# Performance work log

Hardware: AMD Instinct MI355X
Metric: run time of the kernel (lower is better)

The kernel has to match this reference:

```python
import jax, jax.numpy as jnp
import numpy as np

B, S, D, K = 4, 8192, 512, 20


def setup_inputs() -> dict:
    key = jax.random.key(0)
    k1, k2, k3, k4 = jax.random.split(key, 4)
    std = 0.02  # _init_weights: normal(0, 0.02/sqrt(layer_idx+1)), layer_idx=0
    return {
        "x": jax.random.normal(k1, (B, S, D), dtype=jnp.float32),
        "positions": jax.random.normal(k2, (K, D), dtype=jnp.float32) * 0.2,
        "log_scales": jnp.log(1.0 + 0.5 * jax.random.uniform(k3, (K,), dtype=jnp.float32)),
        "amplitudes": 1.2 + 0.3 * jax.random.uniform(k4, (K,), dtype=jnp.float32),
        "w_v": jax.random.normal(jax.random.fold_in(key, 10), (D, D), dtype=jnp.float32) * std,
        "w_o": jax.random.normal(jax.random.fold_in(key, 11), (D, D), dtype=jnp.float32) * std,
    }


def reference(x, positions, log_scales, amplitudes, w_v, w_o):
    # Gaussian-splat RBF attention (token -> splat -> token routing).
    scales = jnp.exp(log_scales)  # [K]
    # squared distances ||x - c||^2 via expansion (avoids [B,S,K,D] tensor)
    x2 = jnp.sum(x * x, axis=-1, keepdims=True)           # [B,S,1]
    c2 = jnp.sum(positions * positions, axis=-1)          # [K]
    xc = jnp.einsum('bsd,kd->bsk', x, positions)          # [B,S,K]
    d2 = jnp.maximum(x2 - 2.0 * xc + c2, 0.0)             # [B,S,K]
    gauss = amplitudes * jnp.exp(-0.5 * d2 / (scales * scales))  # [B,S,K]
    attn = gauss / (jnp.sum(gauss, axis=-1, keepdims=True) + 1e-8)  # per-token normalize
    v = jnp.einsum('bsd,ed->bse', x, w_v)                 # token_value_proj (no bias)
    splat_states = jnp.einsum('bsk,bsd->bkd', attn, v)    # gather token values at splats
    out = jnp.einsum('bsk,bkd->bsd', attn, splat_states)  # scatter back to tokens
    return jnp.einsum('bsd,ed->bse', out, w_o)            # output_proj (dropout=eval identity)
```

## Files before the change

kernel.cpp:

```cpp
#include <hip/hip_runtime.h>
#include <hip/hip_bf16.h>

#define BB 4
#define SS 8192
#define DD 512
#define KK 20

__device__ __forceinline__ float dot4(float4 a, float4 b) {
  return a.x * b.x + a.y * b.y + a.z * b.z + a.w * b.w;
}

__global__ void k0_params(const float* __restrict__ pos,
                          const float* __restrict__ log_scales,
                          const float* __restrict__ amps,
                          float* __restrict__ params) {
  int k = blockIdx.x;
  int lane = threadIdx.x;
  float acc = 0.f;
  for (int d = lane; d < DD; d += 64) { float p = pos[k * DD + d]; acc += p * p; }
#pragma unroll
  for (int off = 32; off > 0; off >>= 1) acc += __shfl_xor(acc, off);
  if (lane == 0) {
    params[k] = acc;
    float s = __expf(log_scales[k]);
    params[KK + k] = 0.5f / (s * s);
    params[2 * KK + k] = amps[k];
  }
}

__global__ __launch_bounds__(256) void kA_attn(
    const float* __restrict__ x, const float* __restrict__ pos,
    const float* __restrict__ params, float* __restrict__ attn_g) {
  __shared__ float pos_s[KK * DD];
  __shared__ float prm_s[3 * KK];
  int tid = threadIdx.x;
  for (int i = tid; i < KK * DD / 4; i += 256)
    ((float4*)pos_s)[i] = ((const float4*)pos)[i];
  if (tid < 3 * KK) prm_s[tid] = params[tid];
  __syncthreads();

  int b = blockIdx.x >> 8;
  int c = blockIdx.x & 255;
  size_t row0 = (size_t)b * SS + (size_t)c * 32;
  int g = tid >> 4;
  int dsub = tid & 15;

  const float* xA = x + (row0 + g) * DD;
  const float* xB = xA + 16 * DD;

  float accA[KK], accB[KK], x2A = 0.f, x2B = 0.f;
#pragma unroll
  for (int k = 0; k < KK; ++k) { accA[k] = 0.f; accB[k] = 0.f; }

#pragma unroll 2
  for (int j = 0; j < 8; ++j) {
    int d0 = j * 64 + dsub * 4;
    float4 xa = *(const float4*)(xA + d0);
    float4 xb = *(const float4*)(xB + d0);
    x2A += dot4(xa, xa);
    x2B += dot4(xb, xb);
#pragma unroll
    for (int k = 0; k < KK; ++k) {
      float4 p = *(const float4*)(pos_s + k * DD + d0);
      accA[k] += dot4(xa, p);
      accB[k] += dot4(xb, p);
    }
  }

#pragma unroll
  for (int m = 1; m <= 8; m <<= 1) { x2A += __shfl_xor(x2A, m); x2B += __shfl_xor(x2B, m); }
#pragma unroll
  for (int k = 0; k < KK; ++k) {
#pragma unroll
    for (int m = 1; m <= 8; m <<= 1) {
      accA[k] += __shfl_xor(accA[k], m);
      accB[k] += __shfl_xor(accB[k], m);
    }
  }

  if (dsub == 0) {
    float gg[KK];
    float sum = 0.f;
#pragma unroll
    for (int k = 0; k < KK; ++k) {
      float d2 = fmaxf(x2A - 2.f * accA[k] + prm_s[k], 0.f);
      gg[k] = prm_s[2 * KK + k] * __expf(-prm_s[KK + k] * d2);
      sum += gg[k];
    }
    float inv = 1.f / (sum + 1e-8f);
    float* ar = attn_g + (row0 + g) * KK;
#pragma unroll
    for (int k = 0; k < KK; ++k) ar[k] = gg[k] * inv;

    sum = 0.f;
#pragma unroll
    for (int k = 0; k < KK; ++k) {
      float d2 = fmaxf(x2B - 2.f * accB[k] + prm_s[k], 0.f);
      gg[k] = prm_s[2 * KK + k] * __expf(-prm_s[KK + k] * d2);
      sum += gg[k];
    }
    inv = 1.f / (sum + 1e-8f);
    ar = attn_g + (row0 + g + 16) * KK;
#pragma unroll
    for (int k = 0; k < KK; ++k) ar[k] = gg[k] * inv;
  }
}

__global__ __launch_bounds__(256) void kB_scatter(
    const float* __restrict__ x, const float* __restrict__ attn,
    float* __restrict__ Mpart, int tpc) {
  int t = threadIdx.x;
  int c = blockIdx.x;
  int b = blockIdx.y;
  int cpb = gridDim.x;
  size_t row0 = (size_t)b * SS + (size_t)c * tpc;

  float2 Ml[KK];
#pragma unroll
  for (int k = 0; k < KK; ++k) Ml[k] = make_float2(0.f, 0.f);

  const float* xb = x + row0 * DD + 2 * t;
  const float* ab = attn + row0 * KK;
  for (int s = 0; s < tpc; ++s) {
    float2 xv = *(const float2*)(xb + (size_t)s * DD);
    const float4* ar4 = (const float4*)(ab + s * KK);
#pragma unroll
    for (int kk = 0; kk < KK / 4; ++kk) {
      float4 a4 = ar4[kk];
      Ml[4 * kk + 0].x += a4.x * xv.x; Ml[4 * kk + 0].y += a4.x * xv.y;
      Ml[4 * kk + 1].x += a4.y * xv.x; Ml[4 * kk + 1].y += a4.y * xv.y;
      Ml[4 * kk + 2].x += a4.z * xv.x; Ml[4 * kk + 2].y += a4.z * xv.y;
      Ml[4 * kk + 3].x += a4.w * xv.x; Ml[4 * kk + 3].y += a4.w * xv.y;
    }
  }
  float* mp = Mpart + ((size_t)b * cpb + c) * KK * DD + 2 * t;
#pragma unroll
  for (int k = 0; k < KK; ++k) *(float2*)(mp + (size_t)k * DD) = Ml[k];
}

__global__ __launch_bounds__(512) void k3f(
    const float* __restrict__ Mpart, const float* __restrict__ w_v,
    const float* __restrict__ w_o, float* __restrict__ ws2, int cpb) {
  __shared__ float m_s[DD];
  __shared__ float v_s[DD];
  int bk = blockIdx.x;
  int b = bk / KK, k = bk - b * KK;
  int e = threadIdx.x;

  const float* mp = Mpart + ((size_t)b * cpb) * KK * DD + (size_t)k * DD + e;
  float acc = 0.f;
#pragma unroll 8
  for (int c = 0; c < cpb; ++c) acc += mp[(size_t)c * KK * DD];
  m_s[e] = acc;
  __syncthreads();

  const float4* wr = (const float4*)(w_v + (size_t)e * DD);
  float a2 = 0.f;
#pragma unroll 4
  for (int j = 0; j < DD / 4; ++j) a2 += dot4(((const float4*)m_s)[j], wr[j]);
  v_s[e] = a2;
  __syncthreads();

  const float4* wr2 = (const float4*)(w_o + (size_t)e * DD);
  float a3 = 0.f;
#pragma unroll 4
  for (int j = 0; j < DD / 4; ++j) a3 += dot4(((const float4*)v_s)[j], wr2[j]);
  ws2[(size_t)bk * DD + e] = a3;
}

__global__ __launch_bounds__(256) void k5_gather(
    const float* __restrict__ attn, const float* __restrict__ ws2,
    float* __restrict__ out) {
  int tid = threadIdx.x;
  int b = blockIdx.x >> 9;
  int sc = blockIdx.x & 511;
  size_t s0 = (size_t)sc * 16;
  int tr = tid >> 7;
  int e4 = tid & 127;

  float4 w[KK];
  const float* wb = ws2 + (size_t)b * KK * DD + e4 * 4;
#pragma unroll
  for (int k = 0; k < KK; ++k) w[k] = *(const float4*)(wb + (size_t)k * DD);

  size_t rowA = (size_t)b * SS + s0 + tr;
  const float* ar = attn + rowA * KK;
  float* orow = out + rowA * DD + e4 * 4;

#pragma unroll 2
  for (int i = 0; i < 8; ++i) {
    const float4* a4 = (const float4*)(ar + (size_t)2 * i * KK);
    float4 A = a4[0], Bv = a4[1], C = a4[2], Dv = a4[3], E = a4[4];
    float4 o = make_float4(0.f, 0.f, 0.f, 0.f);
#define ACC(av, kbase) \
    o.x += av * w[kbase].x; o.y += av * w[kbase].y; \
    o.z += av * w[kbase].z; o.w += av * w[kbase].w;
    ACC(A.x, 0)  ACC(A.y, 1)  ACC(A.z, 2)  ACC(A.w, 3)
    ACC(Bv.x, 4) ACC(Bv.y, 5) ACC(Bv.z, 6) ACC(Bv.w, 7)
    ACC(C.x, 8)  ACC(C.y, 9)  ACC(C.z, 10) ACC(C.w, 11)
    ACC(Dv.x, 12) ACC(Dv.y, 13) ACC(Dv.z, 14) ACC(Dv.w, 15)
    ACC(E.x, 16) ACC(E.y, 17) ACC(E.z, 18) ACC(E.w, 19)
#undef ACC
    *(float4*)(orow + (size_t)2 * i * DD) = o;
  }
}

extern "C" void kernel_launch(void* const* d_in, const int* in_sizes, int n_in,
                              void* d_out, int out_size, void* d_ws, size_t ws_size,
                              hipStream_t stream) {
  const float* x   = (const float*)d_in[0];
  const float* pos = (const float*)d_in[1];
  const float* ls  = (const float*)d_in[2];
  const float* am  = (const float*)d_in[3];
  const float* w_v = (const float*)d_in[4];
  const float* w_o = (const float*)d_in[5];
  float* out = (float*)d_out;

  float* ws     = (float*)d_ws;
  float* attn   = ws;
  float* ws2    = attn + (size_t)BB * SS * KK;
  float* params = ws2 + (size_t)BB * KK * DD;
  float* Mpart  = params + 64;

  size_t head_f = (size_t)BB * SS * KK + (size_t)BB * KK * DD + 64;
  int cpb = 256, tpc = 32;
  size_t need = (head_f + (size_t)BB * cpb * KK * DD) * sizeof(float);
  if (ws_size < need) { cpb = 128; tpc = 64; }

  k0_params<<<KK, 64, 0, stream>>>(pos, ls, am, params);
  kA_attn<<<1024, 256, 0, stream>>>(x, pos, params, attn);
  kB_scatter<<<dim3(cpb, BB), 256, 0, stream>>>(x, attn, Mpart, tpc);
  k3f<<<BB * KK, 512, 0, stream>>>(Mpart, w_v, w_o, ws2, cpb);
  k5_gather<<<2048, 256, 0, stream>>>(attn, ws2, out);
}
```

Baseline: 280.8 us.

## Split partial-sum reduction into parallel stage and process four rows per thread in attn

The cross-chunk reduction of the scatter partials, previously done serially by only 80 blocks inside the projection kernel, is split out into a separate wide kernel that reduces groups of 32 chunks into 8 partials. The projection kernel then only sums 8 values. Separately, the attention-weight kernel now handles 64 rows per block with four rows per thread, so each shared-memory centroid load is reused across more rows. This adds a kernel launch and extra workspace traffic, and the larger per-thread accumulator arrays raise register pressure, which may lower occupancy.

```diff
diff --git a/kernel.cpp b/kernel.cpp
--- a/kernel.cpp
+++ b/kernel.cpp
@@ -5,6 +5,8 @@
 #define SS 8192
 #define DD 512
 #define KK 20
+#define GG 8
+#define BKD (BB * KK * DD)
 
 __device__ __forceinline__ float dot4(float4 a, float4 b) {
   return a.x * b.x + a.y * b.y + a.z * b.z + a.w * b.w;
@@ -39,70 +41,66 @@
   if (tid < 3 * KK) prm_s[tid] = params[tid];
   __syncthreads();
 
-  int b = blockIdx.x >> 8;
-  int c = blockIdx.x & 255;
-  size_t row0 = (size_t)b * SS + (size_t)c * 32;
-  int g = tid >> 4;
+  int b = blockIdx.x >> 7;
+  int c = blockIdx.x & 127;
+  size_t row0 = (size_t)b * SS + (size_t)c * 64;
+  int q = tid >> 4;
   int dsub = tid & 15;
 
-  const float* xA = x + (row0 + g) * DD;
-  const float* xB = xA + 16 * DD;
-
-  float accA[KK], accB[KK], x2A = 0.f, x2B = 0.f;
-#pragma unroll
-  for (int k = 0; k < KK; ++k) { accA[k] = 0.f; accB[k] = 0.f; }
+  const float* xq = x + (row0 + q) * DD;
+
+  float acc[4][KK];
+  float x2[4];
+#pragma unroll
+  for (int r = 0; r < 4; ++r) {
+    x2[r] = 0.f;
+#pragma unroll
+    for (int k = 0; k < KK; ++k) acc[r][k] = 0.f;
+  }
 
 #pragma unroll 2
   for (int j = 0; j < 8; ++j) {
     int d0 = j * 64 + dsub * 4;
-    float4 xa = *(const float4*)(xA + d0);
-    float4 xb = *(const float4*)(xB + d0);
-    x2A += dot4(xa, xa);
-    x2B += dot4(xb, xb);
+    float4 xv[4];
+#pragma unroll
+    for (int r = 0; r < 4; ++r) xv[r] = *(const float4*)(xq + (size_t)(r * 16) * DD + d0);
+#pragma unroll
+    for (int r = 0; r < 4; ++r) x2[r] += dot4(xv[r], xv[r]);
 #pragma unroll
     for (int k = 0; k < KK; ++k) {
       float4 p = *(const float4*)(pos_s + k * DD + d0);
-      accA[k] += dot4(xa, p);
-      accB[k] += dot4(xb, p);
-    }
-  }
-
-#pragma unroll
-  for (int m = 1; m <= 8; m <<= 1) { x2A += __shfl_xor(x2A, m); x2B += __shfl_xor(x2B, m); }
-#pragma unroll
-  for (int k = 0; k < KK; ++k) {
-#pragma unroll
-    for (int m = 1; m <= 8; m <<= 1) {
-      accA[k] += __shfl_xor(accA[k], m);
-      accB[k] += __shfl_xor(accB[k], m);
+#pragma unroll
+      for (int r = 0; r < 4; ++r) acc[r][k] += dot4(xv[r], p);
+    }
+  }
+
+#pragma unroll
+  for (int r = 0; r < 4; ++r) {
+#pragma unroll
+    for (int m = 1; m <= 8; m <<= 1) x2[r] += __shfl_xor(x2[r], m);
+#pragma unroll
+    for (int k = 0; k < KK; ++k) {
+#pragma unroll
+      for (int m = 1; m <= 8; m <<= 1) acc[r][k] += __shfl_xor(acc[r][k], m);
     }
   }
 
   if (dsub == 0) {
-    float gg[KK];
-    float sum = 0.f;
-#pragma unroll
-    for (int k = 0; k < KK; ++k) {
-      float d2 = fmaxf(x2A - 2.f * accA[k] + prm_s[k], 0.f);
-      gg[k] = prm_s[2 * KK + k] * __expf(-prm_s[KK + k] * d2);
-      sum += gg[k];
-    }
-    float inv = 1.f / (sum + 1e-8f);
-    float* ar = attn_g + (row0 + g) * KK;
-#pragma unroll
-    for (int k = 0; k < KK; ++k) ar[k] = gg[k] * inv;
-
-    sum = 0.f;
-#pragma unroll
-    for (int k = 0; k < KK; ++k) {
-      float d2 = fmaxf(x2B - 2.f * accB[k] + prm_s[k], 0.f);
-      gg[k] = prm_s[2 * KK + k] * __expf(-prm_s[KK + k] * d2);
-      sum += gg[k];
-    }
-    inv = 1.f / (sum + 1e-8f);
-    ar = attn_g + (row0 + g + 16) * KK;
-#pragma unroll
-    for (int k = 0; k < KK; ++k) ar[k] = gg[k] * inv;
+#pragma unroll
+    for (int r = 0; r < 4; ++r) {
+      float gg[KK];
+      float sum = 0.f;
+#pragma unroll
+      for (int k = 0; k < KK; ++k) {
+        float d2 = fmaxf(x2[r] - 2.f * acc[r][k] + prm_s[k], 0.f);
+        gg[k] = prm_s[2 * KK + k] * __expf(-prm_s[KK + k] * d2);
+        sum += gg[k];
+      }
+      float inv = 1.f / (sum + 1e-8f);
+      float* ar = attn_g + (row0 + q + r * 16) * KK;
+#pragma unroll
+      for (int k = 0; k < KK; ++k) ar[k] = gg[k] * inv;
+    }
   }
 }
 
@@ -138,19 +136,33 @@
   for (int k = 0; k < KK; ++k) *(float2*)(mp + (size_t)k * DD) = Ml[k];
 }
 
-__global__ __launch_bounds__(512) void k3f(
-    const float* __restrict__ Mpart, const float* __restrict__ w_v,
-    const float* __restrict__ w_o, float* __restrict__ ws2, int cpb) {
+__global__ __launch_bounds__(256) void kC1_reduce(
+    const float* __restrict__ Mpart, float* __restrict__ red8,
+    int cpb, int cpg) {
+  int idx = blockIdx.x * 256 + threadIdx.x;
+  int g = idx / BKD;
+  int rem = idx - g * BKD;
+  int b = rem / (KK * DD);
+  int kd = rem - b * (KK * DD);
+  const float* p = Mpart + ((size_t)b * cpb + (size_t)g * cpg) * KK * DD + kd;
+  float acc = 0.f;
+#pragma unroll 8
+  for (int c = 0; c < cpg; ++c) acc += p[(size_t)c * KK * DD];
+  red8[idx] = acc;
+}
+
+__global__ __launch_bounds__(512) void k3f8(
+    const float* __restrict__ red8, const float* __restrict__ w_v,
+    const float* __restrict__ w_o, float* __restrict__ ws2) {
   __shared__ float m_s[DD];
   __shared__ float v_s[DD];
   int bk = blockIdx.x;
-  int b = bk / KK, k = bk - b * KK;
   int e = threadIdx.x;
 
-  const float* mp = Mpart + ((size_t)b * cpb) * KK * DD + (size_t)k * DD + e;
+  const float* p = red8 + (size_t)bk * DD + e;
   float acc = 0.f;
-#pragma unroll 8
-  for (int c = 0; c < cpb; ++c) acc += mp[(size_t)c * KK * DD];
+#pragma unroll
+  for (int g = 0; g < GG; ++g) acc += p[(size_t)g * BKD];
   m_s[e] = acc;
   __syncthreads();
 
@@ -220,16 +232,19 @@
   float* attn   = ws;
   float* ws2    = attn + (size_t)BB * SS * KK;
   float* params = ws2 + (size_t)BB * KK * DD;
-  float* Mpart  = params + 64;
-
-  size_t head_f = (size_t)BB * SS * KK + (size_t)BB * KK * DD + 64;
+  float* red8   = params + 64;
+  float* Mpart  = red8 + (size_t)GG * BKD;
+
+  size_t head_f = (size_t)BB * SS * KK + (size_t)BB * KK * DD + 64 + (size_t)GG * BKD;
   int cpb = 256, tpc = 32;
   size_t need = (head_f + (size_t)BB * cpb * KK * DD) * sizeof(float);
   if (ws_size < need) { cpb = 128; tpc = 64; }
+  int cpg = cpb / GG;
 
   k0_params<<<KK, 64, 0, stream>>>(pos, ls, am, params);
-  kA_attn<<<1024, 256, 0, stream>>>(x, pos, params, attn);
+  kA_attn<<<512, 256, 0, stream>>>(x, pos, params, attn);
   kB_scatter<<<dim3(cpb, BB), 256, 0, stream>>>(x, attn, Mpart, tpc);
-  k3f<<<BB * KK, 512, 0, stream>>>(Mpart, w_v, w_o, ws2, cpb);
+  kC1_reduce<<<(GG * BKD) / 256, 256, 0, stream>>>(Mpart, red8, cpb, cpg);
+  k3f8<<<BB * KK, 512, 0, stream>>>(red8, w_v, w_o, ws2);
   k5_gather<<<2048, 256, 0, stream>>>(attn, ws2, out);
 }
```

Result: slower. 290.9 us (+3.6%).
